# Performance work log

Hardware: AMD Instinct MI355X
Metric: run time of the kernel (lower is better)

The kernel has to match this reference:

```python
import jax, jax.numpy as jnp
import numpy as np
import math

B, NQ, NKV, D, H, KP = 4, 8192, 8192, 256, 8, 256
HD = D // H


def setup_inputs() -> dict:
    key = jax.random.key(0)
    ks = jax.random.split(key, 8)
    s = 1.0 / math.sqrt(D)
    return {
        "x1": jax.random.normal(ks[0], (B, NQ, D), dtype=jnp.float32),
        "x2": jax.random.normal(ks[1], (NKV, D), dtype=jnp.float32),
        "Wq": jax.random.normal(ks[2], (D, D), dtype=jnp.float32) * s,
        "Wk": jax.random.normal(ks[3], (D, D), dtype=jnp.float32) * s,
        "Wv": jax.random.normal(ks[4], (D, D), dtype=jnp.float32) * s,
        "Wo": jax.random.normal(ks[5], (D, D), dtype=jnp.float32) * s,
        "E": jax.random.normal(ks[6], (NKV, KP), dtype=jnp.float32) * (1.0 / math.sqrt(NKV)),
        "F": jax.random.normal(ks[7], (NKV, KP), dtype=jnp.float32) * (1.0 / math.sqrt(NKV)),
    }


def reference(x1, x2, Wq, Wk, Wv, Wo, E, F):
    # x1: [B, NQ, D] queries; x2: [NKV, D] shared cross-attention context
    q = x1 @ Wq                               # [B, NQ, D]
    k = x2 @ Wk                               # [NKV, D]
    v = x2 @ Wv                               # [NKV, D]
    # Linformer low-rank compression along the KV sequence axis
    k_low = jnp.einsum('nd,nk->kd', k, E)     # [KP, D]
    v_low = jnp.einsum('nd,nk->kd', v, F)     # [KP, D]
    qh = q.reshape(B, NQ, H, HD)
    kh = k_low.reshape(KP, H, HD)
    vh = v_low.reshape(KP, H, HD)
    scale = 1.0 / math.sqrt(HD)
    scores = jnp.einsum('bqhd,khd->bhqk', qh, kh) * scale  # [B, H, NQ, KP]
    attn = jax.nn.softmax(scores, axis=-1)
    out = jnp.einsum('bhqk,khd->bqhd', attn, vh)           # [B, NQ, H, HD]
    out = out.reshape(B, NQ, D)
    return out @ Wo
```

## Files before the change

kernel.cpp:

```cpp
#include <hip/hip_runtime.h>
#include <math.h>
#include <stdint.h>


typedef unsigned short ushort_t;
typedef __attribute__((ext_vector_type(8))) short bf16x8;
typedef __attribute__((ext_vector_type(8))) _Float16 f16x8;
typedef __attribute__((ext_vector_type(4))) float f32x4;

__device__ __forceinline__ f32x4 MFMA(bf16x8 a, bf16x8 b, f32x4 c) {
  return __builtin_amdgcn_mfma_f32_16x16x32_bf16(a, b, c, 0, 0, 0);
}
__device__ __forceinline__ f32x4 MFMA_H(f16x8 a, f16x8 b, f32x4 c) {
  return __builtin_amdgcn_mfma_f32_16x16x32_f16(a, b, c, 0, 0, 0);
}
__device__ __forceinline__ ushort_t f2bf(float x) {
  uint32_t u = __float_as_uint(x);
  u += 0x7fffu + ((u >> 16) & 1u);
  return (ushort_t)(u >> 16);
}
__device__ __forceinline__ uint32_t cvt_pk_bf16(float a, float b) {
  uint32_t r;
  asm("v_cvt_pk_bf16_f32 %0, %1, %2" : "=v"(r) : "v"(a), "v"(b));
  return r;
}
#define GLDS(gsrc, ldst)                                                    \
  __builtin_amdgcn_global_load_lds(                                         \
      (const __attribute__((address_space(1))) uint32_t*)(const void*)(gsrc), \
      (__attribute__((address_space(3))) uint32_t*)(void*)(ldst), 16, 0, 0)

#define STAGE_ROW(u) \
  (((((u) >> 2) ^ ((u) >> 4)) & 1) | (((u) >> 2) & 6) | (((u) >> 5) << 3))
#define STAGE_G(u) \
  ((((u) ^ ((u) >> 2) ^ ((u) >> 4)) & 1) | (((((u) >> 1) ^ ((u) >> 3)) & 1) << 1))

__global__ __launch_bounds__(256) void k_prep_all(
    const float* __restrict__ x2, const float* __restrict__ E,
    const float* __restrict__ F, const float* __restrict__ Wq,
    const float* __restrict__ Wk, const float* __restrict__ Wv,
    const float* __restrict__ Wo, _Float16* __restrict__ xt,
    ushort_t* __restrict__ wqt, ushort_t* __restrict__ wot,
    _Float16* __restrict__ wkt, _Float16* __restrict__ wvt) {
  __shared__ float tile[64][65];
  const int t = threadIdx.x;
  const int z = blockIdx.z;
  if (z < 3) {
    const int n0 = blockIdx.x * 64;
    const int c0 = blockIdx.y * 64;
    const float* __restrict__ src = (z == 0) ? x2 : (z == 1) ? E : F;
    _Float16* __restrict__ dst = xt + (size_t)z * 2097152;
    const int rr = t >> 4, cc = (t & 15) * 4;
#pragma unroll
    for (int i = 0; i < 4; ++i) {
      float4 v = *(const float4*)&src[(size_t)(n0 + rr + 16 * i) * 256 + c0 + cc];
      tile[cc + 0][rr + 16 * i] = v.x;
      tile[cc + 1][rr + 16 * i] = v.y;
      tile[cc + 2][rr + 16 * i] = v.z;
      tile[cc + 3][rr + 16 * i] = v.w;
    }
    __syncthreads();
#pragma unroll
    for (int rnd = 0; rnd < 2; ++rnd) {
      const int u = rnd * 256 + t;
      const int c = u >> 3, r0 = (u & 7) * 8;
      f16x8 h;
#pragma unroll
      for (int j = 0; j < 8; ++j) h[j] = (_Float16)tile[c][r0 + j];
      *(f16x8*)&dst[(size_t)(c0 + c) * 8192 + n0 + r0] = h;
    }
  } else {
    if (blockIdx.x >= 16) return;
    const int m = blockIdx.y;
    const float* __restrict__ src = (m == 0) ? Wq : (m == 1) ? Wo
                                  : (m == 2) ? Wk : Wv;
    const int tr = (blockIdx.x >> 2) * 64;
    const int tc = (blockIdx.x & 3) * 64;
    const int rr = t >> 4, cc = (t & 15) * 4;
#pragma unroll
    for (int i = 0; i < 4; ++i) {
      float4 v = *(const float4*)&src[(size_t)(tr + rr + 16 * i) * 256 + tc + cc];
      tile[cc + 0][rr + 16 * i] = v.x;
      tile[cc + 1][rr + 16 * i] = v.y;
      tile[cc + 2][rr + 16 * i] = v.z;
      tile[cc + 3][rr + 16 * i] = v.w;
    }
    __syncthreads();
#pragma unroll
    for (int rnd = 0; rnd < 2; ++rnd) {
      const int u = rnd * 256 + t;
      const int nl = u >> 3, kl = (u & 7) * 8;
      if (m < 2) {
        const float sc = (m == 0) ? 0.25503488f : 1.0f;
        bf16x8 hv;
#pragma unroll
        for (int j = 0; j < 8; ++j) hv[j] = (short)f2bf(tile[nl][kl + j] * sc);
        ushort_t* dst = (m == 0) ? wqt : wot;
        *(bf16x8*)&dst[(size_t)(tc + nl) * 256 + tr + kl] = hv;
      } else {
        f16x8 hv;
#pragma unroll
        for (int j = 0; j < 8; ++j) hv[j] = (_Float16)tile[nl][kl + j];
        _Float16* dst = (m == 2) ? wkt : wvt;
        *(f16x8*)&dst[(size_t)(tc + nl) * 256 + tr + kl] = hv;
      }
    }
  }
}

__global__ __launch_bounds__(256, 3) void k_mega1(
    const float* __restrict__ x1, const _Float16* __restrict__ xt,
    const ushort_t* __restrict__ wqt, ushort_t* __restrict__ Qf,
    float* __restrict__ part) {
  __shared__ __align__(16) char smem[32768];
  const int t = threadIdx.x;
  const int wv = t >> 6, ln = t & 63;
  const int l15 = ln & 15, g = ln >> 4;

  if (blockIdx.x < 512) {
    ushort_t* wstage = (ushort_t*)smem;
    const size_t r0 = (size_t)blockIdx.x * 64;
    auto stage = [&](int row0, int colu, int buf) {
#pragma unroll
      for (int rnd = 0; rnd < 2; ++rnd) {
        const int u = rnd * 256 + wv * 64 + ln;
        const int row = STAGE_ROW(u);
        const int gg = STAGE_G(u);
        GLDS(wqt + (size_t)(row0 + row) * 256 + colu + gg * 8,
             &wstage[(buf * 512 + rnd * 256 + wv * 64) * 8]);
      }
    };
    f32x4 qacc[16];
#pragma unroll
    for (int i = 0; i < 16; ++i) qacc[i] = {0.f, 0.f, 0.f, 0.f};
    stage(0, 0, 0);
    const float* xrow = x1 + (r0 + wv * 16 + l15) * 256;
    float4 xa = *(const float4*)(xrow + g * 8);
    float4 xb = *(const float4*)(xrow + g * 8 + 4);
    __syncthreads();
    for (int ci = 0; ci < 16; ++ci) {
      const int nh = ci & 1;
      if (ci < 15) stage(((ci + 1) & 1) * 128, ((ci + 1) >> 1) * 32, (ci + 1) & 1);
      union { uint32_t u[4]; bf16x8 v; } af;
      af.u[0] = cvt_pk_bf16(xa.x, xa.y);
      af.u[1] = cvt_pk_bf16(xa.z, xa.w);
      af.u[2] = cvt_pk_bf16(xb.x, xb.y);
      af.u[3] = cvt_pk_bf16(xb.z, xb.w);
      const bf16x8 afrag = af.v;
      const ushort_t* cw = &wstage[(ci & 1) * 4096];
#pragma unroll
      for (int tt = 0; tt < 8; ++tt) {
        bf16x8 bfr = *(const bf16x8*)&cw[((tt * 16 + l15) * 32 + g * 8) ^
                                         ((l15 & 7) << 3)];
        qacc[nh * 8 + tt] = MFMA(afrag, bfr, qacc[nh * 8 + tt]);
      }
      if (nh == 1 && ci < 15) {
        int ks = (ci >> 1) + 1;
        xa = *(const float4*)(xrow + ks * 32 + g * 8);
        xb = *(const float4*)(xrow + ks * 32 + g * 8 + 4);
      }
      __syncthreads();
    }
    char* myq = smem + wv * 8192;
#pragma unroll
    for (int tt = 0; tt < 16; ++tt)
#pragma unroll
      for (int r = 0; r < 4; ++r) {
        const int gr = g * 4 + r;
        *(ushort_t*)(myq + gr * 512 + (((tt * 16 + l15) * 2) ^ ((gr & 7) << 4))) =
            f2bf(qacc[tt][r]);
      }
    __builtin_amdgcn_sched_barrier(0);
    const int rt = blockIdx.x * 4 + wv;
#pragma unroll
    for (int hh = 0; hh < 8; ++hh) {
      bf16x8 qf = *(const bf16x8*)(myq + l15 * 512 +
                                   ((hh * 64 + g * 16) ^ ((l15 & 7) << 4)));
      *(bf16x8*)&Qf[((size_t)(rt * 8 + hh) * 64 + ln) * 8] = qf;
    }
  } else {
    const int bid = blockIdx.x - 512;
    const int which = bid & 1;
    const int chunk = (bid >> 1) & 15;
    const int quad = bid >> 5;
    const int kp0 = (quad >> 1) * 128;
    const int d0 = (quad & 1) * 128;
    const int n0 = chunk * 512;
    const _Float16* __restrict__ A = xt + (size_t)(1 + which) * 2097152;
    const _Float16* __restrict__ B = xt;
    const int wr = wv >> 1, wc = wv & 1;
    f32x4 acc[4][4];
#pragma unroll
    for (int i = 0; i < 4; ++i)
#pragma unroll
      for (int j = 0; j < 4; ++j) acc[i][j] = {0.f, 0.f, 0.f, 0.f};

    for (int ks = 0; ks < 8; ++ks) {
#pragma unroll
      for (int r8 = 0; r8 < 8; ++r8) {
        const int u = r8 * 256 + t;
        const int mm = u >> 10;
        const int uu = u & 1023;
        const int row = uu >> 3;
        const int nsw = ((uu ^ row) & 7) << 3;
        const _Float16* gs =
            (mm ? B + (size_t)(d0 + row) * 8192
                : A + (size_t)(kp0 + row) * 8192) +
            n0 + ks * 64 + nsw;
        GLDS(gs, smem + (u & ~63) * 16);
      }
      __syncthreads();
      const char* la = smem;
      const char* lb = smem + 16384;
#pragma unroll
      for (int kk = 0; kk < 2; ++kk) {
        f16x8 af[4], bf[4];
#pragma unroll
        for (int i = 0; i < 4; ++i) {
          const int ra = wr * 64 + i * 16 + l15;
          af[i] = *(const f16x8*)(la + ra * 128 +
                                  ((kk * 64 + g * 16) ^ ((ra & 7) << 4)));
        }
#pragma unroll
        for (int j = 0; j < 4; ++j) {
          const int rb = wc * 64 + j * 16 + l15;
          bf[j] = *(const f16x8*)(lb + rb * 128 +
                                  ((kk * 64 + g * 16) ^ ((rb & 7) << 4)));
        }
#pragma unroll
        for (int i = 0; i < 4; ++i)
#pragma unroll
          for (int j = 0; j < 4; ++j)
            acc[i][j] = MFMA_H(af[i], bf[j], acc[i][j]);
      }
      __syncthreads();
    }
    float* __restrict__ p = part + ((size_t)which * 16 + chunk) * 65536;
#pragma unroll
    for (int i = 0; i < 4; ++i)
#pragma unroll
      for (int j = 0; j < 4; ++j)
#pragma unroll
        for (int r = 0; r < 4; ++r)
          p[(size_t)(kp0 + wr * 64 + i * 16 + g * 4 + r) * 256 + d0 + wc * 64 +
            j * 16 + l15] = acc[i][j][r];
  }
}

__global__ __launch_bounds__(256) void k_reduce_part(
    const float* __restrict__ part, _Float16* __restrict__ ghh) {
  const int oid = blockIdx.x * 256 + threadIdx.x;
  const int which = oid >> 16;
  const int base = oid & 65535;
  const float* __restrict__ p = part + (size_t)which * 16 * 65536 + base;
  float s = 0.f;
#pragma unroll
  for (int c = 0; c < 16; ++c) s += p[c * 65536];
  ghh[oid] = (_Float16)s;
}

__global__ __launch_bounds__(256, 4) void k_lowproj2(
    const _Float16* __restrict__ ghh, const _Float16* __restrict__ wkt,
    const _Float16* __restrict__ wvt, ushort_t* __restrict__ klowA,
    ushort_t* __restrict__ vtb) {
  __shared__ __align__(16) _Float16 wstage[2][4096];
  const int t = threadIdx.x;
  const int wv = t >> 6, ln = t & 63;
  const int l15 = ln & 15, g = ln >> 4;
  const int which = blockIdx.y;
  const int r0 = blockIdx.x * 64;
  const _Float16* __restrict__ A = ghh + (size_t)which * 65536;
  const _Float16* __restrict__ W = which ? wvt : wkt;

  auto stage = [&](int row0, int colu, int buf) {
#pragma unroll
    for (int rnd = 0; rnd < 2; ++rnd) {
      const int u = rnd * 256 + wv * 64 + ln;
      const int row = STAGE_ROW(u);
      const int gg = STAGE_G(u);
      GLDS(W + (size_t)(row0 + row) * 256 + colu + gg * 8,
           &wstage[buf][(rnd * 256 + wv * 64) * 8]);
    }
  };

  f32x4 yacc[16];
#pragma unroll
  for (int i = 0; i < 16; ++i) yacc[i] = {0.f, 0.f, 0.f, 0.f};
  stage(0, 0, 0);
  const _Float16* arow = A + (size_t)(r0 + wv * 16 + l15) * 256;
  __syncthreads();
  for (int ci = 0; ci < 16; ++ci) {
    const int nh = ci & 1, ks = ci >> 1;
    if (ci < 15) stage(((ci + 1) & 1) * 128, ((ci + 1) >> 1) * 32, (ci + 1) & 1);
    f16x8 afrag = *(const f16x8*)(arow + ks * 32 + g * 8);
    const _Float16* cw = wstage[ci & 1];
#pragma unroll
    for (int tt = 0; tt < 8; ++tt) {
      f16x8 bfr = *(const f16x8*)&cw[((tt * 16 + l15) * 32 + g * 8) ^
                                     ((l15 & 7) << 3)];
      yacc[nh * 8 + tt] = MFMA_H(afrag, bfr, yacc[nh * 8 + tt]);
    }
    __syncthreads();
  }
#pragma unroll
  for (int tt = 0; tt < 16; ++tt)
#pragma unroll
    for (int r = 0; r < 4; ++r) {
      const int rowi = r0 + wv * 16 + g * 4 + r;
      const int c = tt * 16 + l15;
      const int hh = c >> 5, d = c & 31;
      const ushort_t val = f2bf(yacc[tt][r]);
      if (which == 0) {
        klowA[(hh << 13) + ((((rowi & 255) << 5) | d) ^ ((rowi & 7) << 3))] = val;
      } else {
        const int kh = (rowi >> 7) & 1, kl = rowi & 127;
        vtb[(((hh * 2 + kh) * 32 + d) << 7) + (kl ^ ((d & 7) << 3))] = val;
      }
    }
}

__global__ __launch_bounds__(512, 4) void k_attn(
    const ushort_t* __restrict__ Qf, const ushort_t* __restrict__ klowA,
    const ushort_t* __restrict__ vtb, ushort_t* __restrict__ O) {
  __shared__ __align__(16) ushort_t kv[16384];
  __shared__ __align__(16) uint32_t p_buf[8][320];
  __shared__ __align__(16) ushort_t o_sl[8][640];
  const int t = threadIdx.x;
  const int wv = t >> 6, ln = t & 63;
  const int l15 = ln & 15, g = ln >> 4;
  const int h = blockIdx.y;
  const size_t r0 = (size_t)blockIdx.x * 256;

  {
    const ushort_t* ksrc = klowA + h * 8192;
    const ushort_t* vsrc = vtb + h * 8192;
#pragma unroll
    for (int rnd = 0; rnd < 2; ++rnd) {
      const int ub = rnd * 512 + wv * 64;
      GLDS(ksrc + (ub + ln) * 8, &kv[ub * 8]);
    }
#pragma unroll
    for (int rnd = 0; rnd < 2; ++rnd) {
      const int ub = rnd * 512 + wv * 64;
      GLDS(vsrc + (ub + ln) * 8, &kv[8192 + ub * 8]);
    }
  }
  const int rtb = blockIdx.x * 16 + wv;
  bf16x8 qfA = *(const bf16x8*)&Qf[((size_t)(rtb * 8 + h) * 64 + ln) * 8];
  bf16x8 qfB = *(const bf16x8*)&Qf[((size_t)((rtb + 8) * 8 + h) * 64 + ln) * 8];
  __syncthreads();

#pragma unroll
  for (int st = 0; st < 2; ++st) {
    const bf16x8 qfrag = st ? qfB : qfA;
    f32x4 s[16];
#pragma unroll
    for (int tt = 0; tt < 16; ++tt) {
      bf16x8 kfr = *(const bf16x8*)&kv[((tt * 16 + l15) * 32 + g * 8) ^
                                       ((l15 & 7) << 3)];
      f32x4 z = {0.f, 0.f, 0.f, 0.f};
      s[tt] = MFMA(kfr, qfrag, z);
    }
    float sum = 0.f;
    uint32_t pw[16][2];
#pragma unroll
    for (int tt = 0; tt < 16; ++tt) {
      float e0 = exp2f(s[tt][0]), e1 = exp2f(s[tt][1]);
      float e2 = exp2f(s[tt][2]), e3 = exp2f(s[tt][3]);
      sum += (e0 + e1) + (e2 + e3);
      pw[tt][0] = cvt_pk_bf16(e0, e1);
      pw[tt][1] = cvt_pk_bf16(e2, e3);
    }
    sum += __shfl_xor(sum, 16);
    sum += __shfl_xor(sum, 32);
    const float rinv = 1.0f / sum;
    float rv[4];
#pragma unroll
    for (int r = 0; r < 4; ++r) rv[r] = __shfl(rinv, g * 4 + r);

    f32x4 oacc[2];
    oacc[0] = {0.f, 0.f, 0.f, 0.f};
    oacc[1] = {0.f, 0.f, 0.f, 0.f};
    uint32_t* pbw = &p_buf[wv][l15 * 20];
#pragma unroll
    for (int kh = 0; kh < 2; ++kh) {
      const char* cv = (const char*)&kv[8192 + kh * 4096];
#pragma unroll
      for (int ksl = 0; ksl < 4; ++ksl) {
        const int ks = kh * 4 + ksl;
        pbw[2 * g + 0] = pw[2 * ks][0];
        pbw[2 * g + 1] = pw[2 * ks][1];
        pbw[8 + 2 * g + 0] = pw[2 * ks + 1][0];
        pbw[8 + 2 * g + 1] = pw[2 * ks + 1][1];
        __builtin_amdgcn_sched_barrier(0);
        bf16x8 pfr = *(const bf16x8*)&p_buf[wv][l15 * 20 + 4 * g];
#pragma unroll
        for (int nt = 0; nt < 2; ++nt) {
          bf16x8 vfr = *(const bf16x8*)(cv + (nt * 16 + l15) * 256 +
                                        ((ksl * 64 + g * 16) ^ ((l15 & 7) << 4)));
          oacc[nt] = MFMA(pfr, vfr, oacc[nt]);
        }
        __builtin_amdgcn_sched_barrier(0);
      }
    }
#pragma unroll
    for (int nt = 0; nt < 2; ++nt)
#pragma unroll
      for (int r = 0; r < 4; ++r)
        o_sl[wv][(g * 4 + r) * 40 + nt * 16 + l15] = f2bf(oacc[nt][r] * rv[r]);
    __builtin_amdgcn_sched_barrier(0);
    {
      const int qr = ln >> 2, d0 = (ln & 3) * 8;
      bf16x8 ov = *(const bf16x8*)&o_sl[wv][qr * 40 + d0];
      *(bf16x8*)&O[(r0 + st * 128 + wv * 16 + qr) * 256 + h * 32 + d0] = ov;
    }
    __builtin_amdgcn_sched_barrier(0);
  }
}

__global__ __launch_bounds__(256, 4) void k_ogemm(
    const ushort_t* __restrict__ O, const ushort_t* __restrict__ wot,
    float* __restrict__ out) {
  __shared__ __align__(16) ushort_t wstage[2][4096];
  const int t = threadIdx.x;
  const int wv = t >> 6, ln = t & 63;
  const int l15 = ln & 15, g = ln >> 4;
  const size_t r0 = (size_t)blockIdx.x * 64;

  auto stage = [&](int row0, int colu, int buf) {
#pragma unroll
    for (int rnd = 0; rnd < 2; ++rnd) {
      const int u = rnd * 256 + wv * 64 + ln;
      const int row = STAGE_ROW(u);
      const int gg = STAGE_G(u);
      GLDS(wot + (size_t)(row0 + row) * 256 + colu + gg * 8,
           &wstage[buf][(rnd * 256 + wv * 64) * 8]);
    }
  };

  f32x4 yacc[16];
#pragma unroll
  for (int i = 0; i < 16; ++i) yacc[i] = {0.f, 0.f, 0.f, 0.f};
  stage(0, 0, 0);
  const ushort_t* arow = O + (r0 + wv * 16 + l15) * 256;
  __syncthreads();
  for (int ci = 0; ci < 16; ++ci) {
    const int nh = ci & 1, ks = ci >> 1;
    if (ci < 15) stage(((ci + 1) & 1) * 128, ((ci + 1) >> 1) * 32, (ci + 1) & 1);
    bf16x8 afrag = *(const bf16x8*)(arow + ks * 32 + g * 8);
    const ushort_t* cw = wstage[ci & 1];
#pragma unroll
    for (int tt = 0; tt < 8; ++tt) {
      bf16x8 bfr = *(const bf16x8*)&cw[((tt * 16 + l15) * 32 + g * 8) ^
                                       ((l15 & 7) << 3)];
      yacc[nh * 8 + tt] = MFMA(afrag, bfr, yacc[nh * 8 + tt]);
    }
    __syncthreads();
  }
#pragma unroll
  for (int tt = 0; tt < 16; ++tt)
#pragma unroll
    for (int r = 0; r < 4; ++r)
      out[(r0 + wv * 16 + g * 4 + r) * 256 + tt * 16 + l15] = yacc[tt][r];
}

extern "C" void kernel_launch(void* const* d_in, const int* in_sizes, int n_in,
                              void* d_out, int out_size, void* d_ws, size_t ws_size,
                              hipStream_t stream) {
  const float* x1 = (const float*)d_in[0];
  const float* x2 = (const float*)d_in[1];
  const float* Wq = (const float*)d_in[2];
  const float* Wk = (const float*)d_in[3];
  const float* Wv = (const float*)d_in[4];
  const float* Wo = (const float*)d_in[5];
  const float* E  = (const float*)d_in[6];
  const float* F  = (const float*)d_in[7];
  float* out = (float*)d_out;
  float* ws = (float*)d_ws;
  _Float16* ghh = (_Float16*)ws;
  ushort_t* wqt = (ushort_t*)(ws + 65536);
  ushort_t* wot = (ushort_t*)(ws + 98304);
  _Float16* wkt = (_Float16*)(ws + 131072);
  _Float16* wvt = (_Float16*)(ws + 163840);
  ushort_t* klowA = (ushort_t*)(ws + 196608);
  ushort_t* vtb = (ushort_t*)(ws + 229376);
  float* part = ws + 262144;
  ushort_t* Qf = (ushort_t*)(ws + 2359296);
  _Float16* xt = (_Float16*)(ws + 6553600);
  ushort_t* O = (ushort_t*)(ws + 6553600);

  k_prep_all<<<dim3(128, 4, 4), 256, 0, stream>>>(x2, E, F, Wq, Wk, Wv, Wo, xt,
                                                  wqt, wot, wkt, wvt);
  k_mega1<<<640, 256, 0, stream>>>(x1, xt, wqt, Qf, part);
  k_reduce_part<<<512, 256, 0, stream>>>(part, ghh);
  k_lowproj2<<<dim3(4, 2), 256, 0, stream>>>(ghh, wkt, wvt, klowA, vtb);
  k_attn<<<dim3(128, 8), 512, 0, stream>>>(Qf, klowA, vtb, O);
  k_ogemm<<<512, 256, 0, stream>>>(O, wot, out);
}
```

Baseline: 83.86 us.

## Fuse partial-sum reduction into low-rank projection kernel via LDS staging

Removes the separate k_reduce_part kernel. k_lowproj2 now sums the 16 fp32 partial chunks directly, converts them to fp16, and stores the A tile in swizzled LDS before the MFMA loop. This drops one launch and the global ghh round-trip, but the 8MB reduction read now runs on only 8 blocks, limiting bandwidth parallelism. The attention kernel's P-buffer writes are also merged into 64-bit LDS stores.

```diff
diff --git a/kernel.cpp b/kernel.cpp
--- a/kernel.cpp
+++ b/kernel.cpp
@@ -246,29 +246,18 @@
   }
 }
 
-__global__ __launch_bounds__(256) void k_reduce_part(
-    const float* __restrict__ part, _Float16* __restrict__ ghh) {
-  const int oid = blockIdx.x * 256 + threadIdx.x;
-  const int which = oid >> 16;
-  const int base = oid & 65535;
-  const float* __restrict__ p = part + (size_t)which * 16 * 65536 + base;
-  float s = 0.f;
-#pragma unroll
-  for (int c = 0; c < 16; ++c) s += p[c * 65536];
-  ghh[oid] = (_Float16)s;
-}
-
-__global__ __launch_bounds__(256, 4) void k_lowproj2(
-    const _Float16* __restrict__ ghh, const _Float16* __restrict__ wkt,
+__global__ __launch_bounds__(256, 2) void k_lowproj2(
+    const float* __restrict__ part, const _Float16* __restrict__ wkt,
     const _Float16* __restrict__ wvt, ushort_t* __restrict__ klowA,
     ushort_t* __restrict__ vtb) {
+  __shared__ __align__(16) _Float16 a_lds[16384];
   __shared__ __align__(16) _Float16 wstage[2][4096];
   const int t = threadIdx.x;
   const int wv = t >> 6, ln = t & 63;
   const int l15 = ln & 15, g = ln >> 4;
   const int which = blockIdx.y;
   const int r0 = blockIdx.x * 64;
-  const _Float16* __restrict__ A = ghh + (size_t)which * 65536;
+  const float* __restrict__ P = part + (size_t)which * 16 * 65536;
   const _Float16* __restrict__ W = which ? wvt : wkt;
 
   auto stage = [&](int row0, int colu, int buf) {
@@ -282,16 +271,34 @@
     }
   };
 
+  stage(0, 0, 0);
+#pragma unroll 4
+  for (int e = 0; e < 16; ++e) {
+    const int u = e * 256 + t;
+    const int row = u >> 6, c4 = u & 63;
+    const float* pp = P + (size_t)(r0 + row) * 256 + c4 * 4;
+    float4 s4 = {0.f, 0.f, 0.f, 0.f};
+#pragma unroll
+    for (int c = 0; c < 16; ++c) {
+      float4 v = *(const float4*)(pp + (size_t)c * 65536);
+      s4.x += v.x; s4.y += v.y; s4.z += v.z; s4.w += v.w;
+    }
+    _Float16 h4[4] = {(_Float16)s4.x, (_Float16)s4.y,
+                      (_Float16)s4.z, (_Float16)s4.w};
+    const int boff = row * 512 + ((c4 * 8) ^ ((row & 7) << 4));
+    *(uint2*)((char*)a_lds + boff) = *(const uint2*)h4;
+  }
+  __syncthreads();
+
   f32x4 yacc[16];
 #pragma unroll
   for (int i = 0; i < 16; ++i) yacc[i] = {0.f, 0.f, 0.f, 0.f};
-  stage(0, 0, 0);
-  const _Float16* arow = A + (size_t)(r0 + wv * 16 + l15) * 256;
-  __syncthreads();
+  const int arow = wv * 16 + l15;
   for (int ci = 0; ci < 16; ++ci) {
     const int nh = ci & 1, ks = ci >> 1;
     if (ci < 15) stage(((ci + 1) & 1) * 128, ((ci + 1) >> 1) * 32, (ci + 1) & 1);
-    f16x8 afrag = *(const f16x8*)(arow + ks * 32 + g * 8);
+    f16x8 afrag = *(const f16x8*)((char*)a_lds + arow * 512 +
+                                  ((ks * 64 + g * 16) ^ ((arow & 7) << 4)));
     const _Float16* cw = wstage[ci & 1];
 #pragma unroll
     for (int tt = 0; tt < 8; ++tt) {
@@ -387,10 +394,11 @@
 #pragma unroll
       for (int ksl = 0; ksl < 4; ++ksl) {
         const int ks = kh * 4 + ksl;
-        pbw[2 * g + 0] = pw[2 * ks][0];
-        pbw[2 * g + 1] = pw[2 * ks][1];
-        pbw[8 + 2 * g + 0] = pw[2 * ks + 1][0];
-        pbw[8 + 2 * g + 1] = pw[2 * ks + 1][1];
+        uint2 w0, w1;
+        w0.x = pw[2 * ks][0];     w0.y = pw[2 * ks][1];
+        w1.x = pw[2 * ks + 1][0]; w1.y = pw[2 * ks + 1][1];
+        *(uint2*)&pbw[2 * g] = w0;
+        *(uint2*)&pbw[8 + 2 * g] = w1;
         __builtin_amdgcn_sched_barrier(0);
         bf16x8 pfr = *(const bf16x8*)&p_buf[wv][l15 * 20 + 4 * g];
 #pragma unroll
@@ -476,7 +484,6 @@
   const float* F  = (const float*)d_in[7];
   float* out = (float*)d_out;
   float* ws = (float*)d_ws;
-  _Float16* ghh = (_Float16*)ws;
   ushort_t* wqt = (ushort_t*)(ws + 65536);
   ushort_t* wot = (ushort_t*)(ws + 98304);
   _Float16* wkt = (_Float16*)(ws + 131072);
@@ -491,8 +498,7 @@
   k_prep_all<<<dim3(128, 4, 4), 256, 0, stream>>>(x2, E, F, Wq, Wk, Wv, Wo, xt,
                                                   wqt, wot, wkt, wvt);
   k_mega1<<<640, 256, 0, stream>>>(x1, xt, wqt, Qf, part);
-  k_reduce_part<<<512, 256, 0, stream>>>(part, ghh);
-  k_lowproj2<<<dim3(4, 2), 256, 0, stream>>>(ghh, wkt, wvt, klowA, vtb);
+  k_lowproj2<<<dim3(4, 2), 256, 0, stream>>>(part, wkt, wvt, klowA, vtb);
   k_attn<<<dim3(128, 8), 512, 0, stream>>>(Qf, klowA, vtb, O);
   k_ogemm<<<512, 256, 0, stream>>>(O, wot, out);
 }
```

Result: slower. 121.9 us (+45.3%).
